# Performance work log

Measured on AMD Instinct MI355X. Metric: run time of the kernel, lower is better.

Reference implementation:

```python
import jax, jax.numpy as jnp
import numpy as np

B, N, D = 2, 2048, 1024
H = 16
D_HEAD = D // H
WINDOW = 128


def setup_inputs() -> dict:
    key = jax.random.key(0)
    ks = jax.random.split(key, 9)
    s = 1.0 / np.sqrt(D)
    return {
        "x": jax.random.normal(ks[0], (B, N, D), dtype=jnp.float32),
        "Wq": jax.random.uniform(ks[1], (D, D), jnp.float32, -s, s),
        "bq": jax.random.uniform(ks[2], (D,), jnp.float32, -s, s),
        "Wk": jax.random.uniform(ks[3], (D, D), jnp.float32, -s, s),
        "bk": jax.random.uniform(ks[4], (D,), jnp.float32, -s, s),
        "Wv": jax.random.uniform(ks[5], (D, D), jnp.float32, -s, s),
        "bv": jax.random.uniform(ks[6], (D,), jnp.float32, -s, s),
        "Wo": jax.random.uniform(ks[7], (D, D), jnp.float32, -s, s),
        "bo": jax.random.uniform(ks[8], (D,), jnp.float32, -s, s),
    }


def reference(x, Wq, bq, Wk, bk, Wv, bv, Wo, bo):
    # Projections (torch Linear: x @ W.T + b), split into heads: (B,H,N,d)
    def proj(W, b):
        y = x @ W.T + b
        return y.reshape(B, N, H, D_HEAD).transpose(0, 2, 1, 3)

    Q = proj(Wq, bq)
    K = proj(Wk, bk)
    V = proj(Wv, bv)

    scale = 1.0 / np.sqrt(D_HEAD)
    scores = jnp.einsum("bhqd,bhkd->bhqk", Q, K) * scale  # (B,H,N,N)

    i = jnp.arange(N)[:, None]
    j = jnp.arange(N)[None, :]
    band = jnp.abs(i - j) <= WINDOW  # (N,N) sliding-window band mask
    scores = jnp.where(band, scores, -jnp.inf)

    probs = jax.nn.softmax(scores, axis=-1)
    out = jnp.einsum("bhqk,bhkd->bhqd", probs, V)  # (B,H,N,d)
    out = out.transpose(0, 2, 1, 3).reshape(B, N, D)
    return out @ Wo.T + bo
```

## Files before the change

### kernel.cpp

```cpp
#include <hip/hip_runtime.h>
#include <hip/hip_bf16.h>
#include <stdint.h>

typedef __bf16 bf16_t;
typedef __bf16 bf16x8 __attribute__((ext_vector_type(8)));
typedef float f32x4 __attribute__((ext_vector_type(4)));

#define NB 2
#define NN 2048
#define ND 1024
#define NH 16
#define DHEAD 64
#define WIN 128

__device__ __forceinline__ void load_lds16(const void* g, void* l) {
  __builtin_amdgcn_global_load_lds(
      (const __attribute__((address_space(1))) uint32_t*)g,
      (__attribute__((address_space(3))) uint32_t*)l, 16, 0, 0);
}

__global__ __launch_bounds__(256)
void cast_all(const float* __restrict__ x,
              const float* __restrict__ Wq, const float* __restrict__ Wk,
              const float* __restrict__ Wv, const float* __restrict__ Wo,
              bf16_t* __restrict__ xb,
              bf16_t* __restrict__ Wqb, bf16_t* __restrict__ Wkb,
              bf16_t* __restrict__ Wvb, bf16_t* __restrict__ Wob) {
  int i = blockIdx.x * 256 + threadIdx.x;
  const float* in;
  bf16_t* out;
  int off;
  if (i < 1048576) {
    in = x; out = xb; off = i;
  } else {
    int j = i - 1048576;
    int wsel = j >> 18;
    off = j & 262143;
    in  = (wsel == 0) ? Wq  : (wsel == 1) ? Wk  : (wsel == 2) ? Wv  : Wo;
    out = (wsel == 0) ? Wqb : (wsel == 1) ? Wkb : (wsel == 2) ? Wvb : Wob;
  }
  float4 v = reinterpret_cast<const float4*>(in)[off];
  union { bf16_t h[4]; uint2 u; } o;
  o.h[0] = (bf16_t)v.x; o.h[1] = (bf16_t)v.y;
  o.h[2] = (bf16_t)v.z; o.h[3] = (bf16_t)v.w;
  reinterpret_cast<uint2*>(out)[off] = o.u;
}

__global__ __launch_bounds__(512, 6)
void qkv_gemm(const bf16_t* __restrict__ xb,
              const bf16_t* __restrict__ Wqb, const bf16_t* __restrict__ Wkb,
              const bf16_t* __restrict__ Wvb,
              const float* __restrict__ bq, const float* __restrict__ bk,
              const float* __restrict__ bv,
              bf16_t* __restrict__ Qh, bf16_t* __restrict__ Kh,
              bf16_t* __restrict__ VTt) {
  __shared__ __align__(16) bf16_t As[2 * 4096];
  __shared__ __align__(16) bf16_t Bs[2 * 4096];

  const int z = blockIdx.z;
  const bf16_t* Bw  = (z == 0) ? Wqb : (z == 1) ? Wkb : Wvb;
  const float* bias = (z == 0) ? bq  : (z == 1) ? bk  : bv;
  const int m0 = blockIdx.y * 128, n0 = blockIdx.x * 128;

  const int tid = threadIdx.x, lane = tid & 63, w = tid >> 6;
  const int wm = w >> 2, wn = w & 3;
  const int lrow = lane & 15, lkg = lane >> 4;
  const int rsw = (lrow >> 1) & 3;
  const int sr = lane >> 2;
  const int sc = ((lane & 3) ^ ((lane >> 3) & 3)) * 8;

  const bf16_t* abase = xb + (size_t)(m0 + w * 16 + sr) * 1024 + sc;
  const bf16_t* bbase = Bw + (size_t)(n0 + w * 16 + sr) * 1024 + sc;

  f32x4 acc[4][2] = {};

  auto stage = [&](int buf, int k0) {
    load_lds16(abase + k0, As + buf * 4096 + w * 512);
    load_lds16(bbase + k0, Bs + buf * 4096 + w * 512);
  };

  stage(0, 0);
  __syncthreads();

  for (int t = 0; t < 32; ++t) {
    if (t < 31) stage((t + 1) & 1, (t + 1) << 5);
    const bf16_t* Ab = As + (t & 1) * 4096;
    const bf16_t* Bb = Bs + (t & 1) * 4096;
    bf16x8 af[4], bf[2];
#pragma unroll
    for (int m = 0; m < 4; ++m) {
      const int row = wm * 64 + m * 16 + lrow;
      af[m] = *reinterpret_cast<const bf16x8*>(Ab + row * 32 + ((lkg ^ ((row >> 1) & 3)) << 3));
    }
#pragma unroll
    for (int n = 0; n < 2; ++n) {
      const int row = wn * 32 + n * 16 + lrow;
      bf[n] = *reinterpret_cast<const bf16x8*>(Bb + row * 32 + ((lkg ^ ((row >> 1) & 3)) << 3));
    }
#pragma unroll
    for (int m = 0; m < 4; ++m)
#pragma unroll
      for (int n = 0; n < 2; ++n)
        acc[m][n] = __builtin_amdgcn_mfma_f32_16x16x32_bf16(af[m], bf[n], acc[m][n], 0, 0, 0);
    __syncthreads();
  }

#pragma unroll
  for (int m = 0; m < 4; ++m)
#pragma unroll
    for (int n = 0; n < 2; ++n)
#pragma unroll
      for (int r = 0; r < 4; ++r) {
        int row = m0 + wm * 64 + m * 16 + lkg * 4 + r;
        int col = n0 + wn * 32 + n * 16 + lrow;
        float val = acc[m][n][r] + bias[col];
        int bb = row >> 11, tok = row & 2047;
        int hh = col >> 6,  dd = col & 63;
        if (z == 2) {
          VTt[((((size_t)(bb * NH + hh) * 32 + (tok >> 6)) * 64 + dd) << 6) + (tok & 63)] = (bf16_t)val;
        } else {
          bf16_t* outp = (z == 0) ? Qh : Kh;
          outp[(((size_t)(bb * NH + hh) * NN + tok) << 6) + dd] = (bf16_t)val;
        }
      }
}

__global__ __launch_bounds__(512, 2)
void out_gemm2(const bf16_t* __restrict__ AOb, const bf16_t* __restrict__ Wob,
               const float* __restrict__ bo, float* __restrict__ Cout) {
  __shared__ __align__(16) bf16_t lds[32768];

  const int m0 = blockIdx.y * 128, n0 = blockIdx.x * 128;
  const int tid = threadIdx.x, lane = tid & 63, w = tid >> 6;
  const int g = w >> 2;
  const int pair = w & 3;
  const int wr = pair >> 1, wc = pair & 1;
  const int lrow = lane & 15, lkg = lane >> 4;
  const int rsw = (lrow >> 1) & 3;
  const int srow = lane >> 2;
  const int scol = ((lane & 3) ^ ((lane >> 3) & 3)) * 8;

  const bf16_t* abase = AOb + (size_t)(m0 + srow) * 1024 + g * 512 + scol;
  const bf16_t* bbase = Wob + (size_t)(n0 + srow) * 1024 + g * 512 + scol;

  f32x4 acc[4][4] = {};

  auto stage = [&](int buf, int k0) {
#pragma unroll
    for (int i = 0; i < 2; ++i) {
      const int rbase = (pair * 2 + i) * 16;
      bf16_t* seg = &lds[(g * 2 + buf) * 8192];
      load_lds16(abase + (size_t)rbase * 1024 + k0, seg + rbase * 32);
      load_lds16(bbase + (size_t)rbase * 1024 + k0, seg + 4096 + rbase * 32);
    }
  };

  stage(0, 0);
  __syncthreads();

  for (int t = 0; t < 16; ++t) {
    if (t < 15) stage((t + 1) & 1, (t + 1) << 5);
    const bf16_t* Ab = &lds[(g * 2 + (t & 1)) * 8192];
    const bf16_t* Bb = Ab + 4096;
    bf16x8 af[4], bf[4];
#pragma unroll
    for (int m = 0; m < 4; ++m)
      af[m] = *reinterpret_cast<const bf16x8*>(Ab + (wr * 64 + m * 16 + lrow) * 32 + ((lkg ^ rsw) << 3));
#pragma unroll
    for (int n = 0; n < 4; ++n)
      bf[n] = *reinterpret_cast<const bf16x8*>(Bb + (wc * 64 + n * 16 + lrow) * 32 + ((lkg ^ rsw) << 3));
#pragma unroll
    for (int m = 0; m < 4; ++m)
#pragma unroll
      for (int n = 0; n < 4; ++n)
        acc[m][n] = __builtin_amdgcn_mfma_f32_16x16x32_bf16(af[m], bf[n], acc[m][n], 0, 0, 0);
    __syncthreads();
  }

  float* fl = reinterpret_cast<float*>(lds);
  if (g == 1) {
#pragma unroll
    for (int m = 0; m < 4; ++m)
#pragma unroll
      for (int n = 0; n < 4; ++n)
#pragma unroll
        for (int r = 0; r < 4; ++r)
          fl[pair * 4096 + ((m * 4 + n) * 4 + r) * 64 + lane] = acc[m][n][r];
  }
  __syncthreads();
  if (g == 0) {
#pragma unroll
    for (int m = 0; m < 4; ++m)
#pragma unroll
      for (int n = 0; n < 4; ++n)
#pragma unroll
        for (int r = 0; r < 4; ++r) {
          int row = m0 + wr * 64 + m * 16 + lkg * 4 + r;
          int col = n0 + wc * 64 + n * 16 + lrow;
          float val = acc[m][n][r] + fl[pair * 4096 + ((m * 4 + n) * 4 + r) * 64 + lane] + bo[col];
          Cout[(size_t)row * 1024 + col] = val;
        }
  }
}

__global__ __launch_bounds__(256)
void attn_kernel(const bf16_t* __restrict__ Qh, const bf16_t* __restrict__ Kh,
                 const bf16_t* __restrict__ VTt, bf16_t* __restrict__ AO) {
  __shared__ __align__(16) bf16_t KV_lds[2][2][4096];
  __shared__ uint32_t P_lds[4][16][32];

  const int work = ((blockIdx.x & 7) << 7) | (blockIdx.x >> 3);
  const int qt = work & 31, h = (work >> 5) & 15, b = work >> 9;
  const int tid = threadIdx.x, lane = tid & 63, w = tid >> 6;
  const int lrow = lane & 15, lkg = lane >> 4;
  const int q0 = qt * 64;
  const int qb = q0 + w * 16;
  const int qrow = qb + lrow;
  const int rs7 = lrow & 7;

  const int srow8 = lane >> 3;
  const int sswz  = 8 * ((lane & 7) ^ srow8);

  const bf16_t* kbase = Kh  + ((size_t)(b * NH + h) * NN) * DHEAD;
  const bf16_t* vbase = VTt + ((size_t)(b * NH + h) * (NN / 64)) * DHEAD * 64;

  const bf16_t* qptr = Qh + (((size_t)(b * NH + h) * NN + qrow) << 6) + lkg * 8;
  bf16x8 qf0 = *reinterpret_cast<const bf16x8*>(qptr);
  bf16x8 qf1 = *reinterpret_cast<const bf16x8*>(qptr + 32);

  float m_run = -1e30f, l_run = 0.f;
  f32x4 o[4] = {};

  const int kstart = (q0 - WIN > 0) ? (q0 - WIN) : 0;
  const int kend = (q0 + 64 + WIN < NN) ? (q0 + 64 + WIN) : NN;
  const int nch = (kend - kstart) >> 6;
  const float scale = 0.125f;

  auto stage = [&](int bufi, int kc) {
#pragma unroll
    for (int j = 0; j < 2; ++j) {
      const int i = w * 2 + j;
      load_lds16(kbase + (((size_t)(kc + i * 8 + srow8)) << 6) + sswz,
                 &KV_lds[bufi][0][i * 512]);
      load_lds16(vbase + (((size_t)((kc >> 6) * 64 + i * 8 + srow8)) << 6) + sswz,
                 &KV_lds[bufi][1][i * 512]);
    }
  };

  stage(0, kstart);
  __syncthreads();

  for (int ic = 0; ic < nch; ++ic) {
    const int kc = kstart + ic * 64;
    const int bi = ic & 1;
    if (ic + 1 < nch) stage(bi ^ 1, kc + 64);

    const bf16_t* Kt = &KV_lds[bi][0][0];
    const bf16_t* Vt = &KV_lds[bi][1][0];

    f32x4 s[4];
#pragma unroll
    for (int t = 0; t < 4; ++t) {
      const bf16_t* kr = Kt + (t * 16 + lrow) * 64;
      bf16x8 kf0 = *reinterpret_cast<const bf16x8*>(kr + ((lkg ^ rs7) << 3));
      bf16x8 kf1 = *reinterpret_cast<const bf16x8*>(kr + (((4 + lkg) ^ rs7) << 3));
      f32x4 zz = {};
      zz = __builtin_amdgcn_mfma_f32_16x16x32_bf16(kf0, qf0, zz, 0, 0, 0);
      zz = __builtin_amdgcn_mfma_f32_16x16x32_bf16(kf1, qf1, zz, 0, 0, 0);
      s[t] = zz;
    }

    bf16x8 vf0[4], vf1[4];
#pragma unroll
    for (int f = 0; f < 4; ++f) {
      const bf16_t* vr = Vt + (f * 16 + lrow) * 64;
      vf0[f] = *reinterpret_cast<const bf16x8*>(vr + ((lkg ^ rs7) << 3));
      vf1[f] = *reinterpret_cast<const bf16x8*>(vr + (((4 + lkg) ^ rs7) << 3));
    }

    const bool needs_mask = (kc < qb - 113) || (kc > qb + 65);
    float p[4][4];
    float mloc = -1e30f, rsum = 0.f;
    if (needs_mask) {
      float v[4][4];
#pragma unroll
      for (int t = 0; t < 4; ++t)
#pragma unroll
        for (int r = 0; r < 4; ++r) {
          int k = kc + t * 16 + lkg * 4 + r;
          int d = qrow - k;
          bool ok = (unsigned)(d + WIN) <= 2u * WIN;
          v[t][r] = ok ? s[t][r] * scale : -1e30f;
          mloc = fmaxf(mloc, v[t][r]);
        }
      mloc = fmaxf(mloc, __shfl_xor(mloc, 16, 64));
      mloc = fmaxf(mloc, __shfl_xor(mloc, 32, 64));
      float mn = fmaxf(m_run, mloc);
      float corr = __expf(m_run - mn);
      m_run = mn;
#pragma unroll
      for (int t = 0; t < 4; ++t)
#pragma unroll
        for (int r = 0; r < 4; ++r) {
          int k = kc + t * 16 + lkg * 4 + r;
          int d = qrow - k;
          bool ok = (unsigned)(d + WIN) <= 2u * WIN;
          p[t][r] = ok ? __expf(v[t][r] - mn) : 0.f;
          rsum += p[t][r];
        }
      rsum += __shfl_xor(rsum, 16, 64);
      rsum += __shfl_xor(rsum, 32, 64);
      l_run = l_run * corr + rsum;
#pragma unroll
      for (int f = 0; f < 4; ++f) o[f] *= corr;
    } else {
      float v[4][4];
#pragma unroll
      for (int t = 0; t < 4; ++t)
#pragma unroll
        for (int r = 0; r < 4; ++r) {
          v[t][r] = s[t][r] * scale;
          mloc = fmaxf(mloc, v[t][r]);
        }
      mloc = fmaxf(mloc, __shfl_xor(mloc, 16, 64));
      mloc = fmaxf(mloc, __shfl_xor(mloc, 32, 64));
      float mn = fmaxf(m_run, mloc);
      float corr = __expf(m_run - mn);
      m_run = mn;
#pragma unroll
      for (int t = 0; t < 4; ++t)
#pragma unroll
        for (int r = 0; r < 4; ++r) {
          p[t][r] = __expf(v[t][r] - mn);
          rsum += p[t][r];
        }
      rsum += __shfl_xor(rsum, 16, 64);
      rsum += __shfl_xor(rsum, 32, 64);
      l_run = l_run * corr + rsum;
#pragma unroll
      for (int f = 0; f < 4; ++f) o[f] *= corr;
    }

    uint32_t* prow = &P_lds[w][lrow][0];
#pragma unroll
    for (int t = 0; t < 4; ++t)
#pragma unroll
      for (int c = 0; c < 2; ++c) {
        union { bf16_t hh[2]; uint32_t u; } pk;
        pk.hh[0] = (bf16_t)p[t][2 * c];
        pk.hh[1] = (bf16_t)p[t][2 * c + 1];
        int L = 8 * t + 2 * lkg + c;
        int pos = (((L >> 2) ^ rs7) << 2) | (L & 3);
        prow[pos] = pk.u;
      }
    asm volatile("" ::: "memory");
    const bf16_t* prd = reinterpret_cast<const bf16_t*>(&P_lds[w][lrow][0]);
    bf16x8 pa0 = *reinterpret_cast<const bf16x8*>(prd + ((lkg ^ rs7) << 3));
    bf16x8 pa1 = *reinterpret_cast<const bf16x8*>(prd + (((4 + lkg) ^ rs7) << 3));

#pragma unroll
    for (int f = 0; f < 4; ++f) {
      o[f] = __builtin_amdgcn_mfma_f32_16x16x32_bf16(vf0[f], pa0, o[f], 0, 0, 0);
      o[f] = __builtin_amdgcn_mfma_f32_16x16x32_bf16(vf1[f], pa1, o[f], 0, 0, 0);
    }
    __syncthreads();
  }

  float inv = 1.0f / l_run;
#pragma unroll
  for (int f = 0; f < 4; ++f) {
    union { bf16_t hh[4]; uint2 u; } ov;
#pragma unroll
    for (int r = 0; r < 4; ++r) ov.hh[r] = (bf16_t)(o[f][r] * inv);
    bf16_t* op = AO + (size_t)(b * NN + qrow) * ND + h * DHEAD + f * 16 + lkg * 4;
    *reinterpret_cast<uint2*>(op) = ov.u;
  }
}

extern "C" void kernel_launch(void* const* d_in, const int* in_sizes, int n_in,
                              void* d_out, int out_size, void* d_ws, size_t ws_size,
                              hipStream_t stream) {
  const float* x  = (const float*)d_in[0];
  const float* Wq = (const float*)d_in[1];
  const float* bq = (const float*)d_in[2];
  const float* Wk = (const float*)d_in[3];
  const float* bk = (const float*)d_in[4];
  const float* Wv = (const float*)d_in[5];
  const float* bv = (const float*)d_in[6];
  const float* Wo = (const float*)d_in[7];
  const float* bo = (const float*)d_in[8];
  float* out = (float*)d_out;

  bf16_t* ws  = (bf16_t*)d_ws;
  bf16_t* xb  = ws;
  bf16_t* Wqb = xb  + 4194304;
  bf16_t* Wkb = Wqb + 1048576;
  bf16_t* Wvb = Wkb + 1048576;
  bf16_t* Wob = Wvb + 1048576;
  bf16_t* Qh  = Wob + 1048576;
  bf16_t* Kh  = Qh  + 4194304;
  bf16_t* VTt = Kh  + 4194304;
  bf16_t* AOb = VTt + 4194304;

  cast_all<<<8192, 256, 0, stream>>>(x, Wq, Wk, Wv, Wo, xb, Wqb, Wkb, Wvb, Wob);

  qkv_gemm<<<dim3(8, 32, 3), 512, 0, stream>>>(xb, Wqb, Wkb, Wvb, bq, bk, bv, Qh, Kh, VTt);
  attn_kernel<<<1024, 256, 0, stream>>>(Qh, Kh, VTt, AOb);
  out_gemm2<<<dim3(8, 32), 512, 0, stream>>>(AOb, Wob, bo, out);
}
```

Baseline: 91.91 us.

## Use triple-buffered LDS ring with prefetch distance two in QKV GEMM

Replaces the double-buffered LDS staging in the QKV projection GEMM with a three-slot ring, issuing global-to-LDS loads two k-steps ahead. The full __syncthreads is replaced by manual vmcnt waits plus a raw s_barrier, so loads can stay in flight across iterations. This is meant to hide global memory latency better. In exchange it uses more LDS per block, which can lower occupancy, and the hand-written waitcnt counts carry correctness risk.

```diff
diff --git a/kernel.cpp b/kernel.cpp
--- a/kernel.cpp
+++ b/kernel.cpp
@@ -18,6 +18,8 @@
       (const __attribute__((address_space(1))) uint32_t*)g,
       (__attribute__((address_space(3))) uint32_t*)l, 16, 0, 0);
 }
+
+#define FENCE() asm volatile("" ::: "memory")
 
 __global__ __launch_bounds__(256)
 void cast_all(const float* __restrict__ x,
@@ -54,8 +56,7 @@
               const float* __restrict__ bv,
               bf16_t* __restrict__ Qh, bf16_t* __restrict__ Kh,
               bf16_t* __restrict__ VTt) {
-  __shared__ __align__(16) bf16_t As[2 * 4096];
-  __shared__ __align__(16) bf16_t Bs[2 * 4096];
+  __shared__ __align__(16) bf16_t ring[3][8192];
 
   const int z = blockIdx.z;
   const bf16_t* Bw  = (z == 0) ? Wqb : (z == 1) ? Wkb : Wvb;
@@ -65,7 +66,6 @@
   const int tid = threadIdx.x, lane = tid & 63, w = tid >> 6;
   const int wm = w >> 2, wn = w & 3;
   const int lrow = lane & 15, lkg = lane >> 4;
-  const int rsw = (lrow >> 1) & 3;
   const int sr = lane >> 2;
   const int sc = ((lane & 3) ^ ((lane >> 3) & 3)) * 8;
 
@@ -74,18 +74,21 @@
 
   f32x4 acc[4][2] = {};
 
-  auto stage = [&](int buf, int k0) {
-    load_lds16(abase + k0, As + buf * 4096 + w * 512);
-    load_lds16(bbase + k0, Bs + buf * 4096 + w * 512);
+  auto stage = [&](int t) {
+    const int k0 = t << 5;
+    bf16_t* buf = &ring[t % 3][0];
+    load_lds16(abase + k0, buf + w * 512);
+    load_lds16(bbase + k0, buf + 4096 + w * 512);
   };
 
-  stage(0, 0);
-  __syncthreads();
+  stage(0);
+  stage(1);
+  asm volatile("s_waitcnt vmcnt(2)" ::: "memory");
+  FENCE(); __builtin_amdgcn_s_barrier(); FENCE();
 
   for (int t = 0; t < 32; ++t) {
-    if (t < 31) stage((t + 1) & 1, (t + 1) << 5);
-    const bf16_t* Ab = As + (t & 1) * 4096;
-    const bf16_t* Bb = Bs + (t & 1) * 4096;
+    const bf16_t* Ab = &ring[t % 3][0];
+    const bf16_t* Bb = Ab + 4096;
     bf16x8 af[4], bf[2];
 #pragma unroll
     for (int m = 0; m < 4; ++m) {
@@ -97,12 +100,18 @@
       const int row = wn * 32 + n * 16 + lrow;
       bf[n] = *reinterpret_cast<const bf16x8*>(Bb + row * 32 + ((lkg ^ ((row >> 1) & 3)) << 3));
     }
+    if (t + 2 < 32) stage(t + 2);
 #pragma unroll
     for (int m = 0; m < 4; ++m)
 #pragma unroll
       for (int n = 0; n < 2; ++n)
         acc[m][n] = __builtin_amdgcn_mfma_f32_16x16x32_bf16(af[m], bf[n], acc[m][n], 0, 0, 0);
-    __syncthreads();
+    if (t < 30) {
+      asm volatile("s_waitcnt vmcnt(2)" ::: "memory");
+    } else {
+      asm volatile("s_waitcnt vmcnt(0)" ::: "memory");
+    }
+    FENCE(); __builtin_amdgcn_s_barrier(); FENCE();
   }
 
 #pragma unroll
```

Result: slower. 94.69 us (+3.0%).

## Load K/V fragments directly from global memory in attention, dropping LDS staging

Applied to the files above, without the earlier changes.

The attention kernel no longer stages K and V chunks into double-buffered LDS with async global-to-LDS loads. Each wave now reads its MFMA fragments straight from global memory, and the per-chunk __syncthreads is removed. This cuts LDS usage and block-level synchronisation, which may raise occupancy. The cost is that each of the four waves redundantly fetches the same K/V data through cache, and there is no longer any explicit prefetch overlap.

```diff
diff --git a/kernel.cpp b/kernel.cpp
--- a/kernel.cpp
+++ b/kernel.cpp
@@ -65,7 +65,6 @@
   const int tid = threadIdx.x, lane = tid & 63, w = tid >> 6;
   const int wm = w >> 2, wn = w & 3;
   const int lrow = lane & 15, lkg = lane >> 4;
-  const int rsw = (lrow >> 1) & 3;
   const int sr = lane >> 2;
   const int sc = ((lane & 3) ^ ((lane >> 3) & 3)) * 8;
 
@@ -206,7 +205,6 @@
 __global__ __launch_bounds__(256)
 void attn_kernel(const bf16_t* __restrict__ Qh, const bf16_t* __restrict__ Kh,
                  const bf16_t* __restrict__ VTt, bf16_t* __restrict__ AO) {
-  __shared__ __align__(16) bf16_t KV_lds[2][2][4096];
   __shared__ uint32_t P_lds[4][16][32];
 
   const int work = ((blockIdx.x & 7) << 7) | (blockIdx.x >> 3);
@@ -218,11 +216,8 @@
   const int qrow = qb + lrow;
   const int rs7 = lrow & 7;
 
-  const int srow8 = lane >> 3;
-  const int sswz  = 8 * ((lane & 7) ^ srow8);
-
-  const bf16_t* kbase = Kh  + ((size_t)(b * NH + h) * NN) * DHEAD;
-  const bf16_t* vbase = VTt + ((size_t)(b * NH + h) * (NN / 64)) * DHEAD * 64;
+  const bf16_t* kbase = Kh  + (((size_t)(b * NH + h) * NN) << 6);
+  const bf16_t* vbase = VTt + ((size_t)(b * NH + h) * 32) * 4096;
 
   const bf16_t* qptr = Qh + (((size_t)(b * NH + h) * NN + qrow) << 6) + lkg * 8;
   bf16x8 qf0 = *reinterpret_cast<const bf16x8*>(qptr);
@@ -233,49 +228,28 @@
 
   const int kstart = (q0 - WIN > 0) ? (q0 - WIN) : 0;
   const int kend = (q0 + 64 + WIN < NN) ? (q0 + 64 + WIN) : NN;
-  const int nch = (kend - kstart) >> 6;
   const float scale = 0.125f;
 
-  auto stage = [&](int bufi, int kc) {
-#pragma unroll
-    for (int j = 0; j < 2; ++j) {
-      const int i = w * 2 + j;
-      load_lds16(kbase + (((size_t)(kc + i * 8 + srow8)) << 6) + sswz,
-                 &KV_lds[bufi][0][i * 512]);
-      load_lds16(vbase + (((size_t)((kc >> 6) * 64 + i * 8 + srow8)) << 6) + sswz,
-                 &KV_lds[bufi][1][i * 512]);
-    }
-  };
-
-  stage(0, kstart);
-  __syncthreads();
-
-  for (int ic = 0; ic < nch; ++ic) {
-    const int kc = kstart + ic * 64;
-    const int bi = ic & 1;
-    if (ic + 1 < nch) stage(bi ^ 1, kc + 64);
-
-    const bf16_t* Kt = &KV_lds[bi][0][0];
-    const bf16_t* Vt = &KV_lds[bi][1][0];
-
+  for (int kc = kstart; kc < kend; kc += 64) {
     f32x4 s[4];
 #pragma unroll
     for (int t = 0; t < 4; ++t) {
-      const bf16_t* kr = Kt + (t * 16 + lrow) * 64;
-      bf16x8 kf0 = *reinterpret_cast<const bf16x8*>(kr + ((lkg ^ rs7) << 3));
-      bf16x8 kf1 = *reinterpret_cast<const bf16x8*>(kr + (((4 + lkg) ^ rs7) << 3));
+      const bf16_t* kr = kbase + (((size_t)(kc + t * 16 + lrow)) << 6) + lkg * 8;
+      bf16x8 kf0 = *reinterpret_cast<const bf16x8*>(kr);
+      bf16x8 kf1 = *reinterpret_cast<const bf16x8*>(kr + 32);
       f32x4 zz = {};
       zz = __builtin_amdgcn_mfma_f32_16x16x32_bf16(kf0, qf0, zz, 0, 0, 0);
       zz = __builtin_amdgcn_mfma_f32_16x16x32_bf16(kf1, qf1, zz, 0, 0, 0);
       s[t] = zz;
     }
 
+    const bf16_t* vt = vbase + (size_t)(kc >> 6) * 4096;
     bf16x8 vf0[4], vf1[4];
 #pragma unroll
     for (int f = 0; f < 4; ++f) {
-      const bf16_t* vr = Vt + (f * 16 + lrow) * 64;
-      vf0[f] = *reinterpret_cast<const bf16x8*>(vr + ((lkg ^ rs7) << 3));
-      vf1[f] = *reinterpret_cast<const bf16x8*>(vr + (((4 + lkg) ^ rs7) << 3));
+      const bf16_t* vr = vt + (f * 16 + lrow) * 64 + lkg * 8;
+      vf0[f] = *reinterpret_cast<const bf16x8*>(vr);
+      vf1[f] = *reinterpret_cast<const bf16x8*>(vr + 32);
     }
 
     const bool needs_mask = (kc < qb - 113) || (kc > qb + 65);
@@ -363,7 +337,6 @@
       o[f] = __builtin_amdgcn_mfma_f32_16x16x32_bf16(vf0[f], pa0, o[f], 0, 0, 0);
       o[f] = __builtin_amdgcn_mfma_f32_16x16x32_bf16(vf1[f], pa1, o[f], 0, 0, 0);
     }
-    __syncthreads();
   }
 
   float inv = 1.0f / l_run;
@@ -372,7 +345,7 @@
     union { bf16_t hh[4]; uint2 u; } ov;
 #pragma unroll
     for (int r = 0; r < 4; ++r) ov.hh[r] = (bf16_t)(o[f][r] * inv);
-    bf16_t* op = AO + (size_t)(b * NN + qrow) * ND + h * DHEAD + f * 16 + lkg * 4;
+    bf16_t* op = AO + (size_t)((b * NN + qrow)) * ND + h * DHEAD + f * 16 + lkg * 4;
     *reinterpret_cast<uint2*>(op) = ov.u;
   }
 }
```

New measurement: 119.2 us. 29.7% more time.
